# Kernel optimization log

Measured on AMD Instinct MI355X. Metric: run time of the kernel, lower is better.

The kernel has to match this reference:

```python
import jax, jax.numpy as jnp
import numpy as np

B, N, FD = 2, 50000, 13
E = 250000
M, H = 128, 128          # message_dim, hidden_dim
EDGE_IN = 2 * FD + 8     # 34
NODE_IN = FD + 2 * M     # 269


def _mlp(x, w1, b1, w2, b2):
    return jnp.tanh(x @ w1 + b1) @ w2 + b2


def setup_inputs() -> dict:
    root = jax.random.key(0)
    k = lambda i: jax.random.fold_in(root, i)

    def lin(i, din, dout):
        w = jax.random.normal(k(i), (din, dout), jnp.float32) * np.float32(1.0 / np.sqrt(din))
        b = jax.random.normal(k(i + 100), (dout,), jnp.float32) * np.float32(0.01)
        return w, b

    ew1, eb1 = lin(1, EDGE_IN, H); ew2, eb2 = lin(2, H, M)      # mlp_edge
    ww1, wb1 = lin(3, EDGE_IN, H); ww2, wb2 = lin(4, H, 1)      # mlp_weight
    xw1, xb1 = lin(5, EDGE_IN, H); xw2, xb2 = lin(6, H, M)      # mlp_edge_world
    yw1, yb1 = lin(7, EDGE_IN, H); yw2, yb2 = lin(8, H, 1)      # mlp_weight_world
    nw1, nb1 = lin(9, NODE_IN, H); nw2, nb2 = lin(10, H, FD)    # mlp_node

    z_h = jax.random.normal(k(20), (B, N, FD), jnp.float32)
    edge_hh = jax.random.randint(k(21), (B, 2, E), 0, N, jnp.int32)
    edge_world = jax.random.randint(k(22), (B, 2, E), 0, N, jnp.int32)
    return dict(z_h=z_h, edge_hh=edge_hh, edge_world=edge_world,
                ew1=ew1, eb1=eb1, ew2=ew2, eb2=eb2,
                ww1=ww1, wb1=wb1, ww2=ww2, wb2=wb2,
                xw1=xw1, xb1=xb1, xw2=xw2, xb2=xb2,
                yw1=yw1, yb1=yb1, yw2=yw2, yb2=yb2,
                nw1=nw1, nb1=nb1, nw2=nw2, nb2=nb2)


def _edge_features(z, s, t):
    # z: (N, FD); s, t: (E,)
    pos, vel = z[:, 0:3], z[:, 3:6]
    diff = pos[s] - pos[t]                               # (E, 3)
    dist = jnp.sum(diff * diff, axis=-1, keepdims=True)  # (E, 1) squared distance
    vxc = jnp.cross(vel[s], vel[t])                      # (E, 3)
    vxn = jnp.linalg.norm(vxc, axis=-1, keepdims=True)   # (E, 1)
    return jnp.concatenate([diff, dist, vxc, vxn], axis=-1)  # (E, 8)


def reference(z_h, edge_hh, edge_world,
              ew1, eb1, ew2, eb2, ww1, wb1, ww2, wb2,
              xw1, xb1, xw2, xb2, yw1, yb1, yw2, yb2,
              nw1, nb1, nw2, nb2):
    n_nodes = z_h.shape[1]

    def per_batch(z, e_hh, e_w):
        # normal edges
        s, t = e_hh[0], e_hh[1]
        inp = jnp.concatenate([z[s], z[t], _edge_features(z, s, t)], axis=-1)  # (E, 34)
        m = _mlp(inp, ew1, eb1, ew2, eb2)                                       # (E, M)
        w = jax.nn.sigmoid(_mlp(inp, ww1, wb1, ww2, wb2))                       # (E, 1)
        agg_h = jnp.zeros((n_nodes, M), z.dtype).at[t].add(w * m)
        # world edges
        sw, tw = e_w[0], e_w[1]
        inpw = jnp.concatenate([z[sw], z[tw], _edge_features(z, sw, tw)], axis=-1)
        mw = _mlp(inpw, xw1, xb1, xw2, xb2)
        ww_ = jax.nn.sigmoid(_mlp(inpw, yw1, yb1, yw2, yb2))
        agg_w = jnp.zeros((n_nodes, M), z.dtype).at[tw].add(ww_ * mw)
        return agg_h, agg_w

    m_agg_h, m_agg_w = jax.vmap(per_batch)(z_h, edge_hh, edge_world)  # (B, N, M) each
    input_node = jnp.concatenate([z_h, m_agg_h, m_agg_w], axis=-1)    # (B, N, 269)
    delta_z_h = _mlp(input_node, nw1, nb1, nw2, nb2)                  # (B, N, 13)
    return delta_z_h
```

## Files before the change

### kernel.cpp

```cpp
#include <hip/hip_runtime.h>
#include <hip/hip_bf16.h>

#define B_   2
#define N_   50000
#define FD_  13
#define E_   250000
#define M_   128
#define H_   128

typedef __attribute__((ext_vector_type(8))) short  short8;
typedef __attribute__((ext_vector_type(8))) __bf16 bf16x8;
typedef __attribute__((ext_vector_type(4))) float  f32x4;
typedef __attribute__((ext_vector_type(8))) unsigned short ushort8;

#define AGG_BYTES  (4ull * N_ * 128 * 4)
#define HIST_BYTES (4ull * N_ * 4)
#define SORT_BYTES (4ull * E_ * 4)
#define OFF_EW1 0u
#define OFF_WW1 8192u
#define OFF_EW2 16384u
#define OFF_XW1 32768u
#define OFF_YW1 40960u
#define OFF_XW2 49152u
#define OFF_NW1 65536u
#define OFF_NW2 102400u

__device__ __forceinline__ float bf2f(unsigned short u) {
    unsigned int v = ((unsigned int)u) << 16;
    return __builtin_bit_cast(float, v);
}
__device__ __forceinline__ unsigned short f2bf(float f) {
    __bf16 h = (__bf16)f;
    return __builtin_bit_cast(unsigned short, h);
}
__device__ __forceinline__ float tanh_fast(float x) {
    float e = __expf(x + x);
    float r = __builtin_amdgcn_rcpf(e + 1.0f);
    return __builtin_fmaf(-2.0f, r, 1.0f);
}
__device__ __forceinline__ float sigmoid_fast(float x) {
    return __builtin_amdgcn_rcpf(1.0f + __expf(-x));
}
__device__ __forceinline__ f32x4 mfma16(short8 a, short8 b, f32x4 c) {
    return __builtin_amdgcn_mfma_f32_16x16x32_bf16(
        __builtin_bit_cast(bf16x8, a), __builtin_bit_cast(bf16x8, b), c, 0, 0, 0);
}

__global__ void prep_kernel(const float* __restrict__ ew1, const float* __restrict__ ww1,
                            const float* __restrict__ ew2, const float* __restrict__ xw1,
                            const float* __restrict__ yw1, const float* __restrict__ xw2,
                            const float* __restrict__ nw1, const float* __restrict__ nw2,
                            unsigned short* __restrict__ fb) {
    int m = blockIdx.y, f = blockIdx.x, l = threadIdx.x;
    const float* src; int K, Nn, KS; unsigned int off;
    switch (m) {
        case 0: src = ew1; K = 34;  Nn = 128; KS = 2; off = OFF_EW1; break;
        case 1: src = ww1; K = 34;  Nn = 128; KS = 2; off = OFF_WW1; break;
        case 2: src = ew2; K = 128; Nn = 128; KS = 4; off = OFF_EW2; break;
        case 3: src = xw1; K = 34;  Nn = 128; KS = 2; off = OFF_XW1; break;
        case 4: src = yw1; K = 34;  Nn = 128; KS = 2; off = OFF_YW1; break;
        case 5: src = xw2; K = 128; Nn = 128; KS = 4; off = OFF_XW2; break;
        case 6: src = nw1; K = 269; Nn = 128; KS = 9; off = OFF_NW1; break;
        default: src = nw2; K = 128; Nn = 13; KS = 4; off = OFF_NW2; break;
    }
    int NT = (Nn + 15) / 16;
    if (f >= KS * NT) return;
    int ks = f / NT, nt = f % NT;
    int n = nt * 16 + (l & 15);
    unsigned short* dst = fb + off + ((unsigned int)f * 64u + (unsigned int)l) * 8u;
    #pragma unroll
    for (int j = 0; j < 8; j++) {
        int k = ks * 32 + ((l >> 4) * 8) + j;
        int kk = k; bool valid = (k < K) && (n < Nn);
        if (m == 6) {
            if (k < 256)      kk = k + 13;
            else if (k < 269) kk = k - 256;
            else              valid = false;
            valid = valid && (n < Nn);
        }
        dst[j] = valid ? f2bf(src[kk * Nn + n]) : (unsigned short)0;
    }
}

__global__ void hist_kernel(const int* __restrict__ ehh, const int* __restrict__ eww,
                            int* __restrict__ hist) {
    int p = blockIdx.y, idx = blockIdx.x * 256 + threadIdx.x;
    if (idx >= E_) return;
    const int* eg = ((p >> 1) ? eww : ehh) + (size_t)(p & 1) * 2 * E_;
    atomicAdd(&hist[p * N_ + eg[E_ + idx]], 1);
}

__global__ void scan_kernel(int* __restrict__ hist) {
    __shared__ int part[1024];
    const int p = blockIdx.x, tid = threadIdx.x;
    int* h = hist + p * N_;
    const int lo = tid * 52;
    int cnt = N_ - lo; if (cnt < 0) cnt = 0; if (cnt > 52) cnt = 52;
    int v[52];
    int sum = 0;
    if (cnt == 52) {
        const int4* src = (const int4*)(h + lo);
        #pragma unroll
        for (int i = 0; i < 13; i++) {
            int4 t = src[i];
            v[4*i] = t.x; v[4*i+1] = t.y; v[4*i+2] = t.z; v[4*i+3] = t.w;
        }
        #pragma unroll
        for (int i = 0; i < 52; i++) sum += v[i];
    } else {
        for (int i = 0; i < cnt; i++) sum += h[lo + i];
    }
    part[tid] = sum;
    __syncthreads();
    for (int off = 1; off < 1024; off <<= 1) {
        int t = (tid >= off) ? part[tid - off] : 0;
        __syncthreads();
        part[tid] += t;
        __syncthreads();
    }
    int excl = (tid == 0) ? 0 : part[tid - 1];
    if (cnt == 52) {
        int4* dst = (int4*)(h + lo);
        #pragma unroll
        for (int i = 0; i < 13; i++) {
            int4 o;
            o.x = excl; excl += v[4*i];
            o.y = excl; excl += v[4*i+1];
            o.z = excl; excl += v[4*i+2];
            o.w = excl; excl += v[4*i+3];
            dst[i] = o;
        }
    } else {
        for (int i = 0; i < cnt; i++) { int t = h[lo + i]; h[lo + i] = excl; excl += t; }
    }
}

__global__ void scatter_kernel(const int* __restrict__ ehh, const int* __restrict__ eww,
                               int* __restrict__ hist, unsigned int* __restrict__ sorted) {
    int p = blockIdx.y, idx = blockIdx.x * 256 + threadIdx.x;
    if (idx >= E_) return;
    const int* eg = ((p >> 1) ? eww : ehh) + (size_t)(p & 1) * 2 * E_;
    int s = eg[idx];
    int t = eg[E_ + idx];
    int pos = atomicAdd(&hist[p * N_ + t], 1);
    sorted[(size_t)p * E_ + pos] = (unsigned int)s | ((unsigned int)t << 16);
}

__launch_bounds__(256, 3)
__global__ void edge_kernel_agg(const float* __restrict__ z,
                                const unsigned int* __restrict__ sorted,
                                const unsigned short* __restrict__ fb,
                                float* __restrict__ agg,
                                const float* __restrict__ eb1, const float* __restrict__ wb1,
                                const float* __restrict__ ww2, const float* __restrict__ wb2,
                                const float* __restrict__ eb2,
                                const float* __restrict__ xb1, const float* __restrict__ yb1,
                                const float* __restrict__ yw2, const float* __restrict__ yb2,
                                const float* __restrict__ xb2) {
    __shared__ alignas(16) unsigned short Abuf[128][48];
    __shared__ alignas(16) unsigned short Hbuf[128][136];
    __shared__ float w_acc[128];
    __shared__ int   tgt_s[128];

    const int tid  = threadIdx.x;
    const int lane = tid & 63, wv = tid >> 6, quad = lane >> 4, c = lane & 15;
    const int pass = blockIdx.y, b = pass & 1, set = pass >> 1;
    const int ebase = blockIdx.x * 128;

    const float* zb = z + (size_t)b * N_ * FD_;
    float* aggp = agg + (size_t)pass * N_ * 128;

    const short8* Fm1 = (const short8*)(fb + (set ? OFF_XW1 : OFF_EW1));
    const short8* Fw1 = (const short8*)(fb + (set ? OFF_YW1 : OFF_WW1));
    const short8* Fm2 = (const short8*)(fb + (set ? OFF_XW2 : OFF_EW2));
    const float* B1m = set ? xb1 : eb1;
    const float* B1w = set ? yb1 : wb1;
    const float* B2m = set ? xb2 : eb2;
    const float* Wv2 = set ? yw2 : ww2;
    const float wbias = (set ? yb2 : wb2)[0];

    const int nt0 = wv * 2;
    short8 bm[2][2], bw[2][2], b2f[2][4];
    float bias1m[2], bias1w[2], bias2m[2], w2v[2];
    #pragma unroll
    for (int i = 0; i < 2; i++) {
        int nt = nt0 + i, n = nt * 16 + c;
        #pragma unroll
        for (int ks = 0; ks < 2; ks++) { bm[i][ks] = Fm1[(ks * 8 + nt) * 64 + lane];
                                         bw[i][ks] = Fw1[(ks * 8 + nt) * 64 + lane]; }
        #pragma unroll
        for (int ks = 0; ks < 4; ks++) { b2f[i][ks] = Fm2[(ks * 8 + nt) * 64 + lane]; }
        bias1m[i] = B1m[n]; bias1w[i] = B1w[n];
        bias2m[i] = B2m[n]; w2v[i] = Wv2[n];
    }

    if (tid < 128) {
        const int e = tid;
        const int prt = e >> 4, pqd = (e >> 2) & 3, prr = e & 3;
        const int wpos = pqd * 32 + prt * 4 + prr;
        int sp = ebase + wpos;
        const bool valid = (sp < E_);
        if (!valid) sp = E_ - 1;
        unsigned int st = sorted[(size_t)pass * E_ + sp];
        int s = (int)(st & 0xffffu), t = (int)(st >> 16);
        tgt_s[e] = valid ? t : -1;
        w_acc[e] = 0.0f;
        const float* zs = zb + (size_t)s * 13;
        const float* zt = zb + (size_t)t * 13;
        float fs[13], ft[13];
        __builtin_memcpy(fs, zs, 13 * sizeof(float));
        __builtin_memcpy(ft, zt, 13 * sizeof(float));
        float d0 = fs[0] - ft[0], d1 = fs[1] - ft[1], d2 = fs[2] - ft[2];
        float dist = d0 * d0 + d1 * d1 + d2 * d2;
        float c0 = fs[4] * ft[5] - fs[5] * ft[4];
        float c1 = fs[5] * ft[3] - fs[3] * ft[5];
        float c2 = fs[3] * ft[4] - fs[4] * ft[3];
        float vxn = sqrtf(c0 * c0 + c1 * c1 + c2 * c2);
        unsigned short row[40];
        #pragma unroll
        for (int j = 0; j < 13; j++) { row[j] = f2bf(fs[j]); row[13 + j] = f2bf(ft[j]); }
        row[26] = f2bf(d0); row[27] = f2bf(d1); row[28] = f2bf(d2); row[29] = f2bf(dist);
        row[30] = f2bf(c0); row[31] = f2bf(c1); row[32] = f2bf(c2); row[33] = f2bf(vxn);
        #pragma unroll
        for (int j = 34; j < 40; j++) row[j] = 0;
        #pragma unroll
        for (int v = 0; v < 5; v++) {
            short8 sv;
            #pragma unroll
            for (int j = 0; j < 8; j++) sv[j] = (short)row[v * 8 + j];
            *((short8*)&Abuf[e][v * 8]) = sv;
        }
    }
    __syncthreads();

    #pragma unroll 1
    for (int rt = 0; rt < 8; rt++) {
        const unsigned short* ar = &Abuf[rt * 16 + c][0];
        short8 a0 = *((const short8*)(ar + quad * 8));
        short8 a1 = {};
        if (quad == 0) a1 = *((const short8*)(ar + 32));
        float wpart[4] = {0.f, 0.f, 0.f, 0.f};
        #pragma unroll
        for (int i = 0; i < 2; i++) {
            f32x4 accm = {bias1m[i], bias1m[i], bias1m[i], bias1m[i]};
            f32x4 accw = {bias1w[i], bias1w[i], bias1w[i], bias1w[i]};
            accm = mfma16(a0, bm[i][0], accm);
            accm = mfma16(a1, bm[i][1], accm);
            accw = mfma16(a0, bw[i][0], accw);
            accw = mfma16(a1, bw[i][1], accw);
            int n = (nt0 + i) * 16 + c;
            #pragma unroll
            for (int r = 0; r < 4; r++) {
                Hbuf[rt * 16 + quad * 4 + r][n] = f2bf(tanh_fast(accm[r]));
                wpart[r] += tanh_fast(accw[r]) * w2v[i];
            }
        }
        #pragma unroll
        for (int r = 0; r < 4; r++) {
            float v = wpart[r];
            v += __shfl_xor(v, 1); v += __shfl_xor(v, 2);
            v += __shfl_xor(v, 4); v += __shfl_xor(v, 8);
            if (c == r) atomicAdd(&w_acc[rt * 16 + quad * 4 + r], v);
        }
    }
    __syncthreads();
    if (tid < 128) w_acc[tid] = sigmoid_fast(w_acc[tid] + wbias);
    __syncthreads();

    {
        const int n0 = nt0 * 16 + c;
        const int n1 = n0 + 16;
        int   tp = -1;
        float va0 = 0.f, va1 = 0.f;
        bool  from_start = true;
        #pragma unroll 1
        for (int rt = 0; rt < 8; rt++) {
            const unsigned short* hr = &Hbuf[rt * 16 + c][0];
            short8 h0 = *((const short8*)(hr + quad * 8));
            short8 h1 = *((const short8*)(hr + 32 + quad * 8));
            short8 h2 = *((const short8*)(hr + 64 + quad * 8));
            short8 h3 = *((const short8*)(hr + 96 + quad * 8));
            f32x4 accA = {bias2m[0], bias2m[0], bias2m[0], bias2m[0]};
            f32x4 accB = {bias2m[1], bias2m[1], bias2m[1], bias2m[1]};
            accA = mfma16(h0, b2f[0][0], accA);
            accA = mfma16(h1, b2f[0][1], accA);
            accA = mfma16(h2, b2f[0][2], accA);
            accA = mfma16(h3, b2f[0][3], accA);
            accB = mfma16(h0, b2f[1][0], accB);
            accB = mfma16(h1, b2f[1][1], accB);
            accB = mfma16(h2, b2f[1][2], accB);
            accB = mfma16(h3, b2f[1][3], accB);
            const int elq = rt * 16 + quad * 4;
            #pragma unroll
            for (int r = 0; r < 4; r++) {
                const int row = elq + r;
                const int tg = tgt_s[row];
                const float g = w_acc[row];
                const float v0 = accA[r] * g;
                const float v1 = accB[r] * g;
                if (tg == tp) {
                    va0 += v0; va1 += v1;
                } else {
                    if (tp >= 0) {
                        float* dst = aggp + (size_t)tp * 128;
                        if (from_start) { atomicAdd(dst + n0, va0); atomicAdd(dst + n1, va1); }
                        else            { dst[n0] = va0; dst[n1] = va1; }
                    }
                    tp = tg; va0 = v0; va1 = v1;
                    from_start = (rt == 0 && r == 0);
                }
            }
        }
        if (tp >= 0) {
            float* dst = aggp + (size_t)tp * 128;
            atomicAdd(dst + n0, va0);
            atomicAdd(dst + n1, va1);
        }
    }
}

__launch_bounds__(256, 4)
__global__ void node_fused(const float* __restrict__ z,
                           const float* __restrict__ agg,
                           const unsigned short* __restrict__ fb,
                           const float* __restrict__ nb1,
                           const float* __restrict__ nb2,
                           float* __restrict__ out) {
    __shared__ alignas(16) unsigned short Abuf[16][296];
    __shared__ alignas(16) unsigned short Hbuf[16][136];

    const int tid  = threadIdx.x;
    const int lane = tid & 63, wv = tid >> 6, quad = lane >> 4, c = lane & 15;
    const int g0 = blockIdx.x * 16;

    {
        const int nl = tid >> 4;
        const int part = tid & 15;
        const int g = g0 + nl;
        const int b = (g >= N_) ? 1 : 0;
        const int t = g - b * N_;
        #pragma unroll
        for (int s = 0; s < 2; s++) {
            const float* ap = agg + ((size_t)(s * 2 + b) * N_ + t) * 128 + part * 8;
            f32x4 v0 = *(const f32x4*)(ap);
            f32x4 v1 = *(const f32x4*)(ap + 4);
            ushort8 u;
            #pragma unroll
            for (int k = 0; k < 4; k++) { u[k] = f2bf(v0[k]); u[4 + k] = f2bf(v1[k]); }
            *((ushort8*)&Abuf[nl][s * 128 + part * 8]) = u;
        }
    }
    for (int j = tid; j < 16 * 13; j += 256) {
        int nl = j / 13, k = j % 13;
        Abuf[nl][256 + k] = f2bf(z[(size_t)(g0 + nl) * 13 + k]);
    }
    for (int j = tid; j < 16 * 19; j += 256) {
        int nl = j / 19, k = j % 19;
        Abuf[nl][269 + k] = 0;
    }
    __syncthreads();

    {
        const short8* F1 = (const short8*)(fb + OFF_NW1);
        const int nt0 = wv * 2;
        const float b1a = nb1[nt0 * 16 + c];
        const float b1b = nb1[(nt0 + 1) * 16 + c];
        f32x4 acc0 = {b1a, b1a, b1a, b1a};
        f32x4 acc1 = {b1b, b1b, b1b, b1b};
        #pragma unroll
        for (int ks = 0; ks < 9; ks++) {
            short8 a = *((const short8*)(&Abuf[c][0] + ks * 32 + quad * 8));
            acc0 = mfma16(a, F1[(ks * 8 + nt0) * 64 + lane], acc0);
            acc1 = mfma16(a, F1[(ks * 8 + nt0 + 1) * 64 + lane], acc1);
        }
        #pragma unroll
        for (int r = 0; r < 4; r++) {
            Hbuf[quad * 4 + r][nt0 * 16 + c]       = f2bf(tanh_fast(acc0[r]));
            Hbuf[quad * 4 + r][(nt0 + 1) * 16 + c] = f2bf(tanh_fast(acc1[r]));
        }
    }
    __syncthreads();

    if (wv == 0) {
        const short8* F2 = (const short8*)(fb + OFF_NW2);
        const float bias2 = (c < 13) ? nb2[c] : 0.0f;
        f32x4 acc = {bias2, bias2, bias2, bias2};
        #pragma unroll
        for (int ks = 0; ks < 4; ks++) {
            short8 h = *((const short8*)(&Hbuf[c][0] + ks * 32 + quad * 8));
            acc = mfma16(h, F2[ks * 64 + lane], acc);
        }
        #pragma unroll
        for (int r = 0; r < 4; r++) {
            int g = g0 + quad * 4 + r;
            if (c < 13) out[(size_t)g * 13 + c] = acc[r];
        }
    }
}

extern "C" void kernel_launch(void* const* d_in, const int* in_sizes, int n_in,
                              void* d_out, int out_size, void* d_ws, size_t ws_size,
                              hipStream_t stream) {
    const float* z   = (const float*)d_in[0];
    const int* ehh   = (const int*)d_in[1];
    const int* eww   = (const int*)d_in[2];
    const float* ew1 = (const float*)d_in[3];
    const float* eb1 = (const float*)d_in[4];
    const float* ew2 = (const float*)d_in[5];
    const float* eb2 = (const float*)d_in[6];
    const float* ww1 = (const float*)d_in[7];
    const float* wb1 = (const float*)d_in[8];
    const float* ww2 = (const float*)d_in[9];
    const float* wb2 = (const float*)d_in[10];
    const float* xw1 = (const float*)d_in[11];
    const float* xb1 = (const float*)d_in[12];
    const float* xw2 = (const float*)d_in[13];
    const float* xb2 = (const float*)d_in[14];
    const float* yw1 = (const float*)d_in[15];
    const float* yb1 = (const float*)d_in[16];
    const float* yw2 = (const float*)d_in[17];
    const float* yb2 = (const float*)d_in[18];
    const float* nw1 = (const float*)d_in[19];
    const float* nb1 = (const float*)d_in[20];
    const float* nw2 = (const float*)d_in[21];
    const float* nb2 = (const float*)d_in[22];

    float* agg  = (float*)d_ws;
    int* hist   = (int*)((char*)d_ws + AGG_BYTES);
    unsigned int* sorted = (unsigned int*)((char*)d_ws + AGG_BYTES + HIST_BYTES);
    unsigned short* frag = (unsigned short*)((char*)d_ws + AGG_BYTES + HIST_BYTES + SORT_BYTES);

    hipMemsetAsync(d_ws, 0, AGG_BYTES + HIST_BYTES, stream);
    prep_kernel<<<dim3(72, 8), 64, 0, stream>>>(ew1, ww1, ew2, xw1, yw1, xw2, nw1, nw2, frag);
    hist_kernel<<<dim3((E_ + 255) / 256, 4), 256, 0, stream>>>(ehh, eww, hist);
    scan_kernel<<<4, 1024, 0, stream>>>(hist);
    scatter_kernel<<<dim3((E_ + 255) / 256, 4), 256, 0, stream>>>(ehh, eww, hist, sorted);
    edge_kernel_agg<<<dim3((E_ + 127) / 128, 4), 256, 0, stream>>>(
        z, sorted, frag, agg,
        eb1, wb1, ww2, wb2, eb2,
        xb1, yb1, yw2, yb2, xb2);
    node_fused<<<(B_ * N_) / 16, 256, 0, stream>>>(
        z, agg, frag, nb1, nb2, (float*)d_out);
}
```

Baseline: 433.0 us.

## Fuse workspace zeroing into kernels and halve edge-kernel hidden buffer for occupancy

Drops the separate memset and instead zeroes the histogram inside prep_kernel and the 100 MB aggregation buffer inside scatter_kernel, saving a launch and overlapping the zeroing with other work. The edge kernel now handles its 128-edge tile in two halves of 64 rows, shrinking the shared Hbuf so launch bounds can rise from 3 to 5 blocks per SM. In exchange the edge kernel needs extra barriers, scatter_kernel carries a large grid-stride zeroing loop, and running-sum state is carried across the halves.

```diff
diff --git a/kernel.cpp b/kernel.cpp
--- a/kernel.cpp
+++ b/kernel.cpp
@@ -11,6 +11,7 @@
 typedef __attribute__((ext_vector_type(8))) short  short8;
 typedef __attribute__((ext_vector_type(8))) __bf16 bf16x8;
 typedef __attribute__((ext_vector_type(4))) float  f32x4;
+typedef __attribute__((ext_vector_type(4))) unsigned int uint4v;
 typedef __attribute__((ext_vector_type(8))) unsigned short ushort8;
 
 #define AGG_BYTES  (4ull * N_ * 128 * 4)
@@ -50,8 +51,14 @@
                             const float* __restrict__ ew2, const float* __restrict__ xw1,
                             const float* __restrict__ yw1, const float* __restrict__ xw2,
                             const float* __restrict__ nw1, const float* __restrict__ nw2,
-                            unsigned short* __restrict__ fb) {
+                            unsigned short* __restrict__ fb, uint4v* __restrict__ hist4) {
     int m = blockIdx.y, f = blockIdx.x, l = threadIdx.x;
+    {
+        unsigned int flat = ((unsigned int)m * gridDim.x + (unsigned int)f) * 64u + (unsigned int)l;
+        const uint4v zv = {0u, 0u, 0u, 0u};
+        for (unsigned int i = flat; i < 50000u; i += gridDim.x * gridDim.y * 64u)
+            hist4[i] = zv;
+    }
     const float* src; int K, Nn, KS; unsigned int off;
     switch (m) {
         case 0: src = ew1; K = 34;  Nn = 128; KS = 2; off = OFF_EW1; break;
@@ -136,8 +143,16 @@
 }
 
 __global__ void scatter_kernel(const int* __restrict__ ehh, const int* __restrict__ eww,
-                               int* __restrict__ hist, unsigned int* __restrict__ sorted) {
+                               int* __restrict__ hist, unsigned int* __restrict__ sorted,
+                               uint4v* __restrict__ agg4) {
     int p = blockIdx.y, idx = blockIdx.x * 256 + threadIdx.x;
+    {
+        unsigned int flat = ((unsigned int)p * gridDim.x + (unsigned int)blockIdx.x) * 256u
+                          + (unsigned int)threadIdx.x;
+        const unsigned int nthr = gridDim.x * gridDim.y * 256u;
+        const uint4v zv = {0u, 0u, 0u, 0u};
+        for (unsigned int i = flat; i < 6400000u; i += nthr) agg4[i] = zv;
+    }
     if (idx >= E_) return;
     const int* eg = ((p >> 1) ? eww : ehh) + (size_t)(p & 1) * 2 * E_;
     int s = eg[idx];
@@ -146,7 +161,7 @@
     sorted[(size_t)p * E_ + pos] = (unsigned int)s | ((unsigned int)t << 16);
 }
 
-__launch_bounds__(256, 3)
+__launch_bounds__(256, 5)
 __global__ void edge_kernel_agg(const float* __restrict__ z,
                                 const unsigned int* __restrict__ sorted,
                                 const unsigned short* __restrict__ fb,
@@ -158,7 +173,7 @@
                                 const float* __restrict__ yw2, const float* __restrict__ yb2,
                                 const float* __restrict__ xb2) {
     __shared__ alignas(16) unsigned short Abuf[128][48];
-    __shared__ alignas(16) unsigned short Hbuf[128][136];
+    __shared__ alignas(16) unsigned short Hbuf[64][136];
     __shared__ float w_acc[128];
     __shared__ int   tgt_s[128];
 
@@ -233,49 +248,56 @@
     }
     __syncthreads();
 
+    const int n0 = nt0 * 16 + c;
+    const int n1 = n0 + 16;
+    int   tp = -1;
+    float va0 = 0.f, va1 = 0.f;
+    bool  from_start = true;
+
     #pragma unroll 1
-    for (int rt = 0; rt < 8; rt++) {
-        const unsigned short* ar = &Abuf[rt * 16 + c][0];
-        short8 a0 = *((const short8*)(ar + quad * 8));
-        short8 a1 = {};
-        if (quad == 0) a1 = *((const short8*)(ar + 32));
-        float wpart[4] = {0.f, 0.f, 0.f, 0.f};
-        #pragma unroll
-        for (int i = 0; i < 2; i++) {
-            f32x4 accm = {bias1m[i], bias1m[i], bias1m[i], bias1m[i]};
-            f32x4 accw = {bias1w[i], bias1w[i], bias1w[i], bias1w[i]};
-            accm = mfma16(a0, bm[i][0], accm);
-            accm = mfma16(a1, bm[i][1], accm);
-            accw = mfma16(a0, bw[i][0], accw);
-            accw = mfma16(a1, bw[i][1], accw);
-            int n = (nt0 + i) * 16 + c;
+    for (int half = 0; half < 2; half++) {
+        #pragma unroll 1
+        for (int rti = 0; rti < 4; rti++) {
+            const int rt = half * 4 + rti;
+            const unsigned short* ar = &Abuf[rt * 16 + c][0];
+            short8 a0 = *((const short8*)(ar + quad * 8));
+            short8 a1 = {};
+            if (quad == 0) a1 = *((const short8*)(ar + 32));
+            float wpart[4] = {0.f, 0.f, 0.f, 0.f};
+            #pragma unroll
+            for (int i = 0; i < 2; i++) {
+                f32x4 accm = {bias1m[i], bias1m[i], bias1m[i], bias1m[i]};
+                f32x4 accw = {bias1w[i], bias1w[i], bias1w[i], bias1w[i]};
+                accm = mfma16(a0, bm[i][0], accm);
+                accm = mfma16(a1, bm[i][1], accm);
+                accw = mfma16(a0, bw[i][0], accw);
+                accw = mfma16(a1, bw[i][1], accw);
+                int n = (nt0 + i) * 16 + c;
+                #pragma unroll
+                for (int r = 0; r < 4; r++) {
+                    Hbuf[rti * 16 + quad * 4 + r][n] = f2bf(tanh_fast(accm[r]));
+                    wpart[r] += tanh_fast(accw[r]) * w2v[i];
+                }
+            }
             #pragma unroll
             for (int r = 0; r < 4; r++) {
-                Hbuf[rt * 16 + quad * 4 + r][n] = f2bf(tanh_fast(accm[r]));
-                wpart[r] += tanh_fast(accw[r]) * w2v[i];
+                float v = wpart[r];
+                v += __shfl_xor(v, 1); v += __shfl_xor(v, 2);
+                v += __shfl_xor(v, 4); v += __shfl_xor(v, 8);
+                if (c == r) atomicAdd(&w_acc[rt * 16 + quad * 4 + r], v);
             }
         }
-        #pragma unroll
-        for (int r = 0; r < 4; r++) {
-            float v = wpart[r];
-            v += __shfl_xor(v, 1); v += __shfl_xor(v, 2);
-            v += __shfl_xor(v, 4); v += __shfl_xor(v, 8);
-            if (c == r) atomicAdd(&w_acc[rt * 16 + quad * 4 + r], v);
-        }
-    }
-    __syncthreads();
-    if (tid < 128) w_acc[tid] = sigmoid_fast(w_acc[tid] + wbias);
-    __syncthreads();
-
-    {
-        const int n0 = nt0 * 16 + c;
-        const int n1 = n0 + 16;
-        int   tp = -1;
-        float va0 = 0.f, va1 = 0.f;
-        bool  from_start = true;
+        __syncthreads();
+        if (tid < 64) {
+            int row = half * 64 + tid;
+            w_acc[row] = sigmoid_fast(w_acc[row] + wbias);
+        }
+        __syncthreads();
+
         #pragma unroll 1
-        for (int rt = 0; rt < 8; rt++) {
-            const unsigned short* hr = &Hbuf[rt * 16 + c][0];
+        for (int rti = 0; rti < 4; rti++) {
+            const int rt = half * 4 + rti;
+            const unsigned short* hr = &Hbuf[rti * 16 + c][0];
             short8 h0 = *((const short8*)(hr + quad * 8));
             short8 h1 = *((const short8*)(hr + 32 + quad * 8));
             short8 h2 = *((const short8*)(hr + 64 + quad * 8));
@@ -311,11 +333,12 @@
                 }
             }
         }
-        if (tp >= 0) {
-            float* dst = aggp + (size_t)tp * 128;
-            atomicAdd(dst + n0, va0);
-            atomicAdd(dst + n1, va1);
-        }
+        __syncthreads();
+    }
+    if (tp >= 0) {
+        float* dst = aggp + (size_t)tp * 128;
+        atomicAdd(dst + n0, va0);
+        atomicAdd(dst + n1, va1);
     }
 }
 
@@ -430,11 +453,12 @@
     unsigned int* sorted = (unsigned int*)((char*)d_ws + AGG_BYTES + HIST_BYTES);
     unsigned short* frag = (unsigned short*)((char*)d_ws + AGG_BYTES + HIST_BYTES + SORT_BYTES);
 
-    hipMemsetAsync(d_ws, 0, AGG_BYTES + HIST_BYTES, stream);
-    prep_kernel<<<dim3(72, 8), 64, 0, stream>>>(ew1, ww1, ew2, xw1, yw1, xw2, nw1, nw2, frag);
+    prep_kernel<<<dim3(72, 8), 64, 0, stream>>>(ew1, ww1, ew2, xw1, yw1, xw2, nw1, nw2,
+                                                frag, (uint4v*)hist);
     hist_kernel<<<dim3((E_ + 255) / 256, 4), 256, 0, stream>>>(ehh, eww, hist);
     scan_kernel<<<4, 1024, 0, stream>>>(hist);
-    scatter_kernel<<<dim3((E_ + 255) / 256, 4), 256, 0, stream>>>(ehh, eww, hist, sorted);
+    scatter_kernel<<<dim3((E_ + 255) / 256, 4), 256, 0, stream>>>(ehh, eww, hist, sorted,
+                                                                  (uint4v*)agg);
     edge_kernel_agg<<<dim3((E_ + 127) / 128, 4), 256, 0, stream>>>(
         z, sorted, frag, agg,
         eb1, wb1, ww2, wb2, eb2,
```

After: 587.2 us. +35.6%, slower.
